# Kernel optimization log

Hardware: AMD Instinct MI355X
Metric: run time of the kernel (lower is better)

Reference implementation:

```python
import jax, jax.numpy as jnp
import numpy as np

T, B, D = 2048, 8, 1024
INIT_ALPHA_BIAS = 2.0


def setup_inputs() -> dict:
    key = jax.random.key(0)
    k1, k2, k3, k4 = jax.random.split(key, 4)
    xav = float(np.sqrt(6.0 / (D + D)))  # xavier_uniform bound
    return {
        "x": jax.random.normal(k1, (T, B, D), dtype=jnp.float32),
        "h0": jax.random.normal(k2, (B, D), dtype=jnp.float32),
        "W_alpha": jax.random.uniform(k3, (D, D), jnp.float32, -xav, xav),
        "b_alpha": jnp.full((D,), INIT_ALPHA_BIAS, dtype=jnp.float32),
        "W_v": jax.random.uniform(k4, (D, D), jnp.float32, -xav, xav),
        "b_v": jnp.zeros((D,), dtype=jnp.float32),
    }


def reference(x, h0, W_alpha, b_alpha, W_v, b_v):
    # Gates/values for all timesteps at once (batched GEMMs): [T, B, D]
    alpha = jax.nn.sigmoid(jnp.einsum("tbd,ed->tbe", x, W_alpha) + b_alpha)
    v = jnp.einsum("tbd,ed->tbe", x, W_v) + b_v

    def step(h_prev, av):
        a_t, v_t = av
        h_new = a_t * h_prev + (1.0 - a_t) * v_t
        out_t = h_new * jax.nn.silu(h_new)
        return h_new, (h_new, out_t)

    _, (hs, output) = jax.lax.scan(step, h0, (alpha, v))
    h = jnp.concatenate([h0[None], hs], axis=0)  # [T+1, B, D]
    return output, h
```

## Files before the change

kernel.cpp:

```cpp
#include <hip/hip_runtime.h>
#include <hip/hip_bf16.h>

#define T_DIM 2048
#define B_DIM 8
#define D_DIM 1024
#define M_DIM (T_DIM * B_DIM)
#define K_DIM D_DIM
#define NW_DIM (2 * D_DIM)
#define NCH (B_DIM * D_DIM)
#define NCH4 (NCH / 4)
#define CHUNKS 64
#define CHUNK_LEN 32

typedef __attribute__((ext_vector_type(8))) short bf16x8;
typedef __attribute__((ext_vector_type(4))) float f32x4;

__device__ __forceinline__ unsigned short bf16_rne(float f) {
    unsigned u = __float_as_uint(f);
    unsigned r = u + 0x7fffu + ((u >> 16) & 1u);
    return (unsigned short)(r >> 16);
}

__device__ __forceinline__ float sigmoidf(float z) {
    return 1.0f / (1.0f + __expf(-z));
}

__device__ __forceinline__ void load_lds16(const void* g, void* l) {
    __builtin_amdgcn_global_load_lds(
        (const __attribute__((address_space(1))) void*)g,
        (__attribute__((address_space(3))) void*)l,
        16, 0, 0);
}

__global__ __launch_bounds__(256) void convert_all_kernel(
    const float4* __restrict__ x,
    const float4* __restrict__ Wa,
    const float4* __restrict__ Wv,
    ushort4* __restrict__ xb,
    ushort4* __restrict__ Wcat) {
    const int nx4 = M_DIM * K_DIM / 4;
    const int half4 = D_DIM * D_DIM / 4;
    int i = blockIdx.x * 256 + threadIdx.x;
    float4 f;
    ushort4* __restrict__ dst;
    int di;
    if (i < nx4) {
        f = x[i];
        dst = xb;
        di = i;
    } else {
        int j = i - nx4;
        f = (j < half4) ? Wa[j] : Wv[j - half4];
        dst = Wcat;
        di = j;
    }
    ushort4 o;
    o.x = bf16_rne(f.x);
    o.y = bf16_rne(f.y);
    o.z = bf16_rne(f.z);
    o.w = bf16_rne(f.w);
    dst[di] = o;
}

__global__ __launch_bounds__(512, 4) void gemm_fused_kernel(
    const unsigned short* __restrict__ A,
    const unsigned short* __restrict__ W,
    const float* __restrict__ ba,
    const float* __restrict__ bv,
    float* __restrict__ alpha_dst,
    float* __restrict__ v_dst) {
    extern __shared__ __attribute__((aligned(16))) char smem[];

    const int tid = threadIdx.x;
    const int lane = tid & 63;
    const int w = tid >> 6;
    const int wm = w >> 2;
    const int wn = w & 3;
    const int quad = lane >> 4;
    const int l16 = lane & 15;

    const int bid = blockIdx.x;
    const int swz = (bid & 7) * 128 + (bid >> 3);
    const int bx = swz & 7;
    const int by = swz >> 3;
    const int bm = by * 128;
    const int bn = bx * 256;

    const int vsw = (((l16 & 1) << 2) | quad) ^ (l16 >> 1);
    const int rdA = wm * 4096 + (l16 >> 1) * 128 + vsw * 16;
    const int rdB = wn * 4096 + (l16 >> 1) * 128 + vsw * 16;

    const int hl = lane >> 3;
    const int vp = (lane & 7) ^ hl;
    const int qsrc = vp & 3;
    const int rb = (vp >> 2) & 1;
    const int rA  = 16 * w + 2 * hl + rb;
    const int rB0 = 32 * w + 2 * hl + rb;
    const int rB1 = rB0 + 16;
    const char* Ab = (const char*)A;
    const char* Wb = (const char*)W;
    const size_t offA  = (size_t)(bm + rA ) * 2048 + (size_t)qsrc * 16;
    const size_t offB0 = (size_t)(bn + rB0) * 2048 + (size_t)qsrc * 16;
    const size_t offB1 = (size_t)(bn + rB1) * 2048 + (size_t)qsrc * 16;
    const int ldsA  = w * 1024;
    const int ldsB0 = (2 * w) * 1024;
    const int ldsB1 = (2 * w + 1) * 1024;

    f32x4 acc[4][4];
    {
        f32x4 zero = {0.f, 0.f, 0.f, 0.f};
#pragma unroll
        for (int i = 0; i < 4; ++i)
#pragma unroll
            for (int j = 0; j < 4; ++j) acc[i][j] = zero;
    }

    auto stage = [&](int buf, int t) {
        char* bA = smem + buf * 24576;
        char* bB = bA + 8192;
        const size_t ko = (size_t)t * 64;
        load_lds16(Ab + offA + ko, bA + ldsA);
        load_lds16(Wb + offB0 + ko, bB + ldsB0);
        load_lds16(Wb + offB1 + ko, bB + ldsB1);
    };

    auto tile_step = [&](int buf, int nbuf, int tn, bool do_stage, int vm,
                         bool bar) {
        const char* bA = smem + buf * 24576;
        const char* bB = bA + 8192;
        bf16x8 af[4], bfr[4];
#pragma unroll
        for (int i = 0; i < 4; ++i)
            af[i] = *(const bf16x8*)(bA + rdA + i * 1024);
#pragma unroll
        for (int j = 0; j < 4; ++j)
            bfr[j] = *(const bf16x8*)(bB + rdB + j * 1024);
        if (do_stage) stage(nbuf, tn);
        asm volatile("s_waitcnt lgkmcnt(0)" ::: "memory");
        __builtin_amdgcn_sched_barrier(0);
        __builtin_amdgcn_s_setprio(1);
#pragma unroll
        for (int i = 0; i < 4; ++i)
#pragma unroll
            for (int j = 0; j < 4; ++j)
                acc[i][j] = __builtin_amdgcn_mfma_f32_16x16x32_bf16(
                    af[i], bfr[j], acc[i][j], 0, 0, 0);
        __builtin_amdgcn_s_setprio(0);
        if (vm == 3) asm volatile("s_waitcnt vmcnt(3)" ::: "memory");
        else if (vm == 0) asm volatile("s_waitcnt vmcnt(0)" ::: "memory");
        if (bar) __builtin_amdgcn_s_barrier();
    };

    stage(0, 0);
    stage(1, 1);
    asm volatile("s_waitcnt vmcnt(3)" ::: "memory");
    __builtin_amdgcn_s_barrier();

    for (int it = 0; it < 10; ++it) {
        const int t = it * 3;
        tile_step(0, 2, t + 2, true, 3, true);
        tile_step(1, 0, t + 3, true, 3, true);
        tile_step(2, 1, t + 4, true, 3, true);
    }
    tile_step(0, 0, 0, false, 0, true);
    tile_step(1, 0, 0, false, -1, false);

    const bool is_alpha = (bn < D_DIM);
    float* __restrict__ dst = is_alpha ? alpha_dst : v_dst;
    const float* __restrict__ bias = is_alpha ? ba : bv;
    const int nb = bn - (is_alpha ? 0 : D_DIM);
#pragma unroll
    for (int j = 0; j < 4; ++j) {
        const int n = nb + wn * 64 + j * 16 + l16;
        const float bias_n = bias[n];
#pragma unroll
        for (int i = 0; i < 4; ++i) {
            const int m0 = bm + wm * 64 + i * 16 + quad * 4;
#pragma unroll
            for (int r = 0; r < 4; ++r) {
                float val = acc[i][j][r] + bias_n;
                if (is_alpha) val = sigmoidf(val);
                dst[(size_t)(m0 + r) * D_DIM + n] = val;
            }
        }
    }
}


__global__ __launch_bounds__(256) void scan_phase1_kernel(
    const float4* __restrict__ alpha,
    const float4* __restrict__ v,
    float4* __restrict__ P,
    float4* __restrict__ Q) {
    const int j4 = blockIdx.x * 256 + threadIdx.x;
    const int c = blockIdx.y;
    float4 Pr = {1.f, 1.f, 1.f, 1.f};
    float4 Qr = {0.f, 0.f, 0.f, 0.f};
    size_t base = (size_t)c * CHUNK_LEN * NCH4 + j4;
#pragma unroll 4
    for (int t = 0; t < CHUNK_LEN; ++t) {
        float4 a = alpha[base + (size_t)t * NCH4];
        float4 vv = v[base + (size_t)t * NCH4];
        Pr.x *= a.x; Pr.y *= a.y; Pr.z *= a.z; Pr.w *= a.w;
        Qr.x = a.x * Qr.x + (1.f - a.x) * vv.x;
        Qr.y = a.y * Qr.y + (1.f - a.y) * vv.y;
        Qr.z = a.z * Qr.z + (1.f - a.z) * vv.z;
        Qr.w = a.w * Qr.w + (1.f - a.w) * vv.w;
    }
    P[(size_t)c * NCH4 + j4] = Pr;
    Q[(size_t)c * NCH4 + j4] = Qr;
}

__global__ __launch_bounds__(256) void scan_phase2_kernel(
    const float* __restrict__ P, const float* __restrict__ Q,
    const float* __restrict__ h0,
    float* __restrict__ Hc,
    float* __restrict__ hbase) {
    const int ch = blockIdx.x * 256 + threadIdx.x;
    float h = h0[ch];
    hbase[ch] = h;
#pragma unroll 8
    for (int c = 0; c < CHUNKS; ++c) {
        Hc[(size_t)c * NCH + ch] = h;
        h = P[(size_t)c * NCH + ch] * h + Q[(size_t)c * NCH + ch];
    }
}

__global__ __launch_bounds__(256) void scan_phase3_kernel(
    float4* __restrict__ alpha_out,
    float4* __restrict__ v_h,
    const float4* __restrict__ Hc) {
    const int j4 = blockIdx.x * 256 + threadIdx.x;
    const int c = blockIdx.y;
    float4 h = Hc[(size_t)c * NCH4 + j4];
    size_t base = (size_t)c * CHUNK_LEN * NCH4 + j4;
#pragma unroll 4
    for (int t = 0; t < CHUNK_LEN; ++t) {
        float4 a = alpha_out[base + (size_t)t * NCH4];
        float4 vv = v_h[base + (size_t)t * NCH4];
        h.x = a.x * h.x + (1.f - a.x) * vv.x;
        h.y = a.y * h.y + (1.f - a.y) * vv.y;
        h.z = a.z * h.z + (1.f - a.z) * vv.z;
        h.w = a.w * h.w + (1.f - a.w) * vv.w;
        float4 o;
        o.x = h.x * h.x * sigmoidf(h.x);
        o.y = h.y * h.y * sigmoidf(h.y);
        o.z = h.z * h.z * sigmoidf(h.z);
        o.w = h.w * h.w * sigmoidf(h.w);
        alpha_out[base + (size_t)t * NCH4] = o;
        v_h[base + (size_t)t * NCH4] = h;
    }
}

extern "C" void kernel_launch(void* const* d_in, const int* in_sizes, int n_in,
                              void* d_out, int out_size, void* d_ws, size_t ws_size,
                              hipStream_t stream) {
    const float* x  = (const float*)d_in[0];
    const float* h0 = (const float*)d_in[1];
    const float* Wa = (const float*)d_in[2];
    const float* ba = (const float*)d_in[3];
    const float* Wv = (const float*)d_in[4];
    const float* bv = (const float*)d_in[5];

    float* out = (float*)d_out;
    float* hbase = out + (size_t)T_DIM * NCH;
    float* alpha = out;
    float* vbuf = hbase + NCH;

    char* ws = (char*)d_ws;
    unsigned short* xb   = (unsigned short*)ws;
    unsigned short* Wcat = (unsigned short*)(ws + 33554432);
    float* P  = (float*)(ws + 37748736);
    float* Q  = (float*)(ws + 39845888);
    float* Hc = (float*)(ws + 41943040);

    static bool attr_done = false;
    if (!attr_done) {
        hipFuncSetAttribute(reinterpret_cast<const void*>(gemm_fused_kernel),
                            hipFuncAttributeMaxDynamicSharedMemorySize, 73728);
        attr_done = true;
    }

    const int nconv = (M_DIM * K_DIM / 4) + (2 * D_DIM * D_DIM / 4);
    convert_all_kernel<<<nconv / 256, 256, 0, stream>>>(
        (const float4*)x, (const float4*)Wa, (const float4*)Wv,
        (ushort4*)xb, (ushort4*)Wcat);

    gemm_fused_kernel<<<1024, 512, 73728, stream>>>(xb, Wcat, ba, bv, alpha,
                                                    vbuf);

    dim3 sgrid(NCH4 / 256, CHUNKS);
    scan_phase1_kernel<<<sgrid, 256, 0, stream>>>(
        (const float4*)alpha, (const float4*)vbuf, (float4*)P, (float4*)Q);
    scan_phase2_kernel<<<NCH / 256, 256, 0, stream>>>(
        P, Q, h0, Hc, hbase);
    scan_phase3_kernel<<<sgrid, 256, 0, stream>>>(
        (float4*)alpha, (float4*)vbuf, (const float4*)Hc);
}
```

Baseline: 315.8 us.

## Pack alpha and v into one 32-bit word to halve scan traffic

The GEMM epilogue now stores alpha as 16-bit unsigned fixed point and v as bf16, interleaved into a single 32-bit word per element in the output buffer. The scan phases each load one uint4 instead of two float4s and decode both values. Phase 3 writes h to its own output region. This cuts the bytes the GEMM writes and the scan kernels read for the intermediate gates. In exchange it loses precision on alpha and v, and the GEMM epilogue now issues narrower, strided 2-byte stores.

After: 305.3 us. -3.3%, faster.

```diff
diff --git a/kernel.cpp b/kernel.cpp
--- a/kernel.cpp
+++ b/kernel.cpp
@@ -23,6 +23,11 @@
 
 __device__ __forceinline__ float sigmoidf(float z) {
     return 1.0f / (1.0f + __expf(-z));
+}
+
+__device__ __forceinline__ void decode_av(unsigned u, float& a, float& v) {
+    a = (float)(u & 0xffffu) * (1.0f / 65535.f);
+    v = __uint_as_float(u & 0xffff0000u);
 }
 
 __device__ __forceinline__ void load_lds16(const void* g, void* l) {
@@ -67,8 +72,7 @@
     const unsigned short* __restrict__ W,
     const float* __restrict__ ba,
     const float* __restrict__ bv,
-    float* __restrict__ alpha_dst,
-    float* __restrict__ v_dst) {
+    unsigned short* __restrict__ av) {
     extern __shared__ __attribute__((aligned(16))) char smem[];
 
     const int tid = threadIdx.x;
@@ -166,9 +170,9 @@
     tile_step(1, 0, 0, false, -1, false);
 
     const bool is_alpha = (bn < D_DIM);
-    float* __restrict__ dst = is_alpha ? alpha_dst : v_dst;
     const float* __restrict__ bias = is_alpha ? ba : bv;
     const int nb = bn - (is_alpha ? 0 : D_DIM);
+    const int sel = is_alpha ? 0 : 1;
 #pragma unroll
     for (int j = 0; j < 4; ++j) {
         const int n = nb + wn * 64 + j * 16 + l16;
@@ -179,8 +183,12 @@
 #pragma unroll
             for (int r = 0; r < 4; ++r) {
                 float val = acc[i][j][r] + bias_n;
-                if (is_alpha) val = sigmoidf(val);
-                dst[(size_t)(m0 + r) * D_DIM + n] = val;
+                unsigned short s;
+                if (is_alpha)
+                    s = (unsigned short)(sigmoidf(val) * 65535.f + 0.5f);
+                else
+                    s = bf16_rne(val);
+                av[((size_t)(m0 + r) * D_DIM + n) * 2 + sel] = s;
             }
         }
     }
@@ -188,8 +196,7 @@
 
 
 __global__ __launch_bounds__(256) void scan_phase1_kernel(
-    const float4* __restrict__ alpha,
-    const float4* __restrict__ v,
+    const uint4* __restrict__ av,
     float4* __restrict__ P,
     float4* __restrict__ Q) {
     const int j4 = blockIdx.x * 256 + threadIdx.x;
@@ -199,13 +206,17 @@
     size_t base = (size_t)c * CHUNK_LEN * NCH4 + j4;
 #pragma unroll 4
     for (int t = 0; t < CHUNK_LEN; ++t) {
-        float4 a = alpha[base + (size_t)t * NCH4];
-        float4 vv = v[base + (size_t)t * NCH4];
-        Pr.x *= a.x; Pr.y *= a.y; Pr.z *= a.z; Pr.w *= a.w;
-        Qr.x = a.x * Qr.x + (1.f - a.x) * vv.x;
-        Qr.y = a.y * Qr.y + (1.f - a.y) * vv.y;
-        Qr.z = a.z * Qr.z + (1.f - a.z) * vv.z;
-        Qr.w = a.w * Qr.w + (1.f - a.w) * vv.w;
+        uint4 u = av[base + (size_t)t * NCH4];
+        float a0, v0, a1, v1, a2, v2, a3, v3;
+        decode_av(u.x, a0, v0);
+        decode_av(u.y, a1, v1);
+        decode_av(u.z, a2, v2);
+        decode_av(u.w, a3, v3);
+        Pr.x *= a0; Pr.y *= a1; Pr.z *= a2; Pr.w *= a3;
+        Qr.x = a0 * Qr.x + (1.f - a0) * v0;
+        Qr.y = a1 * Qr.y + (1.f - a1) * v1;
+        Qr.z = a2 * Qr.z + (1.f - a2) * v2;
+        Qr.w = a3 * Qr.w + (1.f - a3) * v3;
     }
     P[(size_t)c * NCH4 + j4] = Pr;
     Q[(size_t)c * NCH4 + j4] = Qr;
@@ -227,8 +238,8 @@
 }
 
 __global__ __launch_bounds__(256) void scan_phase3_kernel(
-    float4* __restrict__ alpha_out,
-    float4* __restrict__ v_h,
+    uint4* __restrict__ av_out,
+    float4* __restrict__ hout,
     const float4* __restrict__ Hc) {
     const int j4 = blockIdx.x * 256 + threadIdx.x;
     const int c = blockIdx.y;
@@ -236,19 +247,23 @@
     size_t base = (size_t)c * CHUNK_LEN * NCH4 + j4;
 #pragma unroll 4
     for (int t = 0; t < CHUNK_LEN; ++t) {
-        float4 a = alpha_out[base + (size_t)t * NCH4];
-        float4 vv = v_h[base + (size_t)t * NCH4];
-        h.x = a.x * h.x + (1.f - a.x) * vv.x;
-        h.y = a.y * h.y + (1.f - a.y) * vv.y;
-        h.z = a.z * h.z + (1.f - a.z) * vv.z;
-        h.w = a.w * h.w + (1.f - a.w) * vv.w;
-        float4 o;
-        o.x = h.x * h.x * sigmoidf(h.x);
-        o.y = h.y * h.y * sigmoidf(h.y);
-        o.z = h.z * h.z * sigmoidf(h.z);
-        o.w = h.w * h.w * sigmoidf(h.w);
-        alpha_out[base + (size_t)t * NCH4] = o;
-        v_h[base + (size_t)t * NCH4] = h;
+        uint4 u = av_out[base + (size_t)t * NCH4];
+        float a0, v0, a1, v1, a2, v2, a3, v3;
+        decode_av(u.x, a0, v0);
+        decode_av(u.y, a1, v1);
+        decode_av(u.z, a2, v2);
+        decode_av(u.w, a3, v3);
+        h.x = a0 * h.x + (1.f - a0) * v0;
+        h.y = a1 * h.y + (1.f - a1) * v1;
+        h.z = a2 * h.z + (1.f - a2) * v2;
+        h.w = a3 * h.w + (1.f - a3) * v3;
+        uint4 o;
+        o.x = __float_as_uint(h.x * h.x * sigmoidf(h.x));
+        o.y = __float_as_uint(h.y * h.y * sigmoidf(h.y));
+        o.z = __float_as_uint(h.z * h.z * sigmoidf(h.z));
+        o.w = __float_as_uint(h.w * h.w * sigmoidf(h.w));
+        av_out[base + (size_t)t * NCH4] = o;
+        hout[((size_t)c * CHUNK_LEN + t + 1) * NCH4 + j4] = h;
     }
 }
 
@@ -264,8 +279,7 @@
 
     float* out = (float*)d_out;
     float* hbase = out + (size_t)T_DIM * NCH;
-    float* alpha = out;
-    float* vbuf = hbase + NCH;
+    unsigned short* av = (unsigned short*)out;
 
     char* ws = (char*)d_ws;
     unsigned short* xb   = (unsigned short*)ws;
@@ -286,14 +300,13 @@
         (const float4*)x, (const float4*)Wa, (const float4*)Wv,
         (ushort4*)xb, (ushort4*)Wcat);
 
-    gemm_fused_kernel<<<1024, 512, 73728, stream>>>(xb, Wcat, ba, bv, alpha,
-                                                    vbuf);
+    gemm_fused_kernel<<<1024, 512, 73728, stream>>>(xb, Wcat, ba, bv, av);
 
     dim3 sgrid(NCH4 / 256, CHUNKS);
     scan_phase1_kernel<<<sgrid, 256, 0, stream>>>(
-        (const float4*)alpha, (const float4*)vbuf, (float4*)P, (float4*)Q);
+        (const uint4*)out, (float4*)P, (float4*)Q);
     scan_phase2_kernel<<<NCH / 256, 256, 0, stream>>>(
         P, Q, h0, Hc, hbase);
     scan_phase3_kernel<<<sgrid, 256, 0, stream>>>(
-        (float4*)alpha, (float4*)vbuf, (const float4*)Hc);
-}
+        (uint4*)out, (float4*)hbase, (const float4*)Hc);
+}
```
